# Performance work log

Hardware: AMD Instinct MI355X
Metric: run time of the kernel (lower is better)

The kernel has to match this reference:

```python
import jax, jax.numpy as jnp
import numpy as np

# Module constants (match init_kwargs / DCNv4 defaults)
N, C, H, W = 4, 256, 128, 128
G = 4                       # DCNv4 default group
KS = 3                      # kernel_size
K = KS * KS                 # 9 sampling points per group
Cg = C // G                 # channels per group
PAD_OFF = int(np.ceil(G * K * 3 / 8) * 8)  # 112, padded offset_mask dim
EPS = 1e-5                  # BatchNorm2d eps


def setup_inputs() -> dict:
    key = jax.random.key(0)
    ks = jax.random.split(key, 6)
    s = 0.05
    return {
        "x": jax.random.normal(ks[0], (N, C, H, W), jnp.float32),
        "conv_w": jax.random.normal(ks[1], (C, C, 1, 1), jnp.float32) * s,
        "bn1_gamma": jnp.ones((C,), jnp.float32),
        "bn1_beta": jnp.zeros((C,), jnp.float32),
        "bn1_mean": jnp.zeros((C,), jnp.float32),
        "bn1_var": jnp.ones((C,), jnp.float32),
        "value_w": jax.random.normal(ks[2], (C, C), jnp.float32) * s,
        "value_b": jnp.zeros((C,), jnp.float32),
        "offset_w": jax.random.normal(ks[3], (PAD_OFF, C), jnp.float32) * s,
        "offset_b": jnp.zeros((PAD_OFF,), jnp.float32),
        "out_w": jax.random.normal(ks[4], (C, C), jnp.float32) * s,
        "out_b": jnp.zeros((C,), jnp.float32),
        "bn2_gamma": jnp.ones((C,), jnp.float32),
        "bn2_beta": jnp.zeros((C,), jnp.float32),
        "bn2_mean": jnp.zeros((C,), jnp.float32),
        "bn2_var": jnp.ones((C,), jnp.float32),
    }


def _bilinear(v, lh, lw):
    """Bilinear sample v:(N,H,W,G,Cg) at float locs lh/lw:(N,H,W,G); zero outside."""
    n, h, w, g, c = v.shape
    h0 = jnp.floor(lh)
    w0 = jnp.floor(lw)
    dh = lh - h0
    dw = lw - w0
    h0i = h0.astype(jnp.int32)
    w0i = w0.astype(jnp.int32)
    vf = v.reshape(n, h * w, g, c)

    def gather(hh, ww):
        valid = (hh >= 0) & (hh < h) & (ww >= 0) & (ww < w)
        idx = jnp.clip(hh, 0, h - 1) * w + jnp.clip(ww, 0, w - 1)
        out = jnp.take_along_axis(vf, idx.reshape(n, h * w, g)[..., None], axis=1)
        return out.reshape(n, h, w, g, c) * valid[..., None].astype(v.dtype)

    w00 = (1 - dh) * (1 - dw)
    w01 = (1 - dh) * dw
    w10 = dh * (1 - dw)
    w11 = dh * dw
    return (gather(h0i, w0i) * w00[..., None]
            + gather(h0i, w0i + 1) * w01[..., None]
            + gather(h0i + 1, w0i) * w10[..., None]
            + gather(h0i + 1, w0i + 1) * w11[..., None])


def _bn(x_nchw, gamma, beta, mean, var):
    scale = (gamma / jnp.sqrt(var + EPS))[None, :, None, None]
    return x_nchw * scale + (beta - mean * gamma / jnp.sqrt(var + EPS))[None, :, None, None]


def reference(x, conv_w, bn1_gamma, bn1_beta, bn1_mean, bn1_var,
              value_w, value_b, offset_w, offset_b, out_w, out_b,
              bn2_gamma, bn2_beta, bn2_mean, bn2_var):
    n, _, h, w = x.shape
    # ---- Conv(c1,c2,k=1): 1x1 conv (no bias) + BN + SiLU ----
    y = jnp.einsum('nchw,oc->nohw', x, conv_w[:, :, 0, 0])
    y = jax.nn.silu(_bn(y, bn1_gamma, bn1_beta, bn1_mean, bn1_var))

    # ---- DCNv4 on (N, L, C) tokens ----
    t = y.transpose(0, 2, 3, 1)                      # (N,H,W,C)
    v = t @ value_w.T + value_b                      # value_proj
    om = t @ offset_w.T + offset_b                   # (N,H,W,112)
    om = om[..., : G * K * 3].reshape(n, h, w, G, K * 3)
    off = om[..., : 2 * K].reshape(n, h, w, G, K, 2) # (dx, dy) per point
    mask = om[..., 2 * K:]                           # (N,H,W,G,K), no softmax in v4
    v = v.reshape(n, h, w, G, Cg)

    hi = jnp.arange(h, dtype=jnp.float32)[None, :, None, None]
    wi = jnp.arange(w, dtype=jnp.float32)[None, None, :, None]
    out = jnp.zeros_like(v)
    for k in range(K):  # fixed small kernel loop (9 points)
        i, j = divmod(k, KS)
        lh = hi + (i - 1) + off[..., k, 1]           # stride=1, pad=1, dil=1
        lw = wi + (j - 1) + off[..., k, 0]           # offset_scale=1.0
        out = out + mask[..., k, None] * _bilinear(v, lh, lw)

    o = out.reshape(n, h, w, C) @ out_w.T + out_b    # output_proj
    o = o.transpose(0, 3, 1, 2)                      # back to NCHW

    # ---- final BN + SiLU ----
    return jax.nn.silu(_bn(o, bn2_gamma, bn2_beta, bn2_mean, bn2_var))
```

## Files before the change

### kernel.cpp

```cpp
#include <hip/hip_runtime.h>
#include <cstdint>

typedef unsigned short u16;
typedef unsigned int   u32;
typedef __attribute__((ext_vector_type(8))) __bf16 bf16x8;
typedef __attribute__((ext_vector_type(2))) float  f32x2;
typedef __attribute__((ext_vector_type(4))) float  f32x4;
typedef __attribute__((ext_vector_type(4))) u32    u32x4;

#define N_IMG 4
#define C_DIM 256
#define H_DIM 128
#define W_DIM 128
#define HW    (H_DIM * W_DIM)
#define M_TOT (N_IMG * HW)
#define CG    64
#define PADOFF 112
#define NCAT  368
#define EPSV  1e-5f

__device__ __forceinline__ u16 f2b(float f) {
  u32 u = __float_as_uint(f);
  u += 0x7fffu + ((u >> 16) & 1u);
  return (u16)(u >> 16);
}

__device__ __forceinline__ void async_cp16(const void* g, void* l) {
  __builtin_amdgcn_global_load_lds(
      (const __attribute__((address_space(1))) void*)g,
      (__attribute__((address_space(3))) void*)l, 16, 0, 0);
}

__global__ __launch_bounds__(256) void cast_all(
    const float* __restrict__ a0, u16* __restrict__ o0,
    const float* __restrict__ a1, u16* __restrict__ o1,
    const float* __restrict__ a2, u16* __restrict__ o2,
    const float* __restrict__ a3, u16* __restrict__ o3) {
  int i = blockIdx.x * 256 + threadIdx.x;
  const float* in; u16* out; int base;
  if (i < 16384)      { in = a0; out = o0; base = 0; }
  else if (i < 32768) { in = a1; out = o1; base = 16384; }
  else if (i < 39936) { in = a2; out = o2; base = 32768; }
  else                { in = a3; out = o3; base = 39936; }
  int j = i - base;
  f32x4 v = reinterpret_cast<const f32x4*>(in)[j];
  u32 lo = (u32)f2b(v[0]) | ((u32)f2b(v[1]) << 16);
  u32 hi = (u32)f2b(v[2]) | ((u32)f2b(v[3]) << 16);
  reinterpret_cast<u32*>(out)[2 * j]     = lo;
  reinterpret_cast<u32*>(out)[2 * j + 1] = hi;
}

__global__ __launch_bounds__(256) void fused_proj(
    const float* __restrict__ X, const u16* __restrict__ Bc,
    const u16* __restrict__ Wcat,
    u16* __restrict__ Vv, float* __restrict__ Om,
    const float* __restrict__ vbias, const float* __restrict__ obias,
    const float* __restrict__ gamma, const float* __restrict__ beta,
    const float* __restrict__ mean, const float* __restrict__ var) {
  constexpr int BM = 128, BK = 32;
  __shared__ __align__(16) u16 T[BM * C_DIM];
  __shared__ __align__(16) u16 As[BM * BK];
  __shared__ __align__(16) u16 Bs[BM * BK];
  const int tid  = threadIdx.x;
  const int lane = tid & 63;
  const int wave = tid >> 6;
  const int quad = lane >> 4;
  const int l16  = lane & 15;
  const int bm = blockIdx.x * BM;
  const int wm = (wave & 1) * 64;
  const int wn = (wave >> 1) * 64;
  const int img = bm >> 14;
  const int hw0 = bm & (HW - 1);
  const int p2  = (tid & 63) * 2;
  const int hh  = tid >> 6;
  const float* xb = X + (size_t)img * C_DIM * HW + hw0 + p2;

  for (int ny = 0; ny < 2; ++ny) {
    const int bn = ny * 128;
    f32x4 acc[4][4] = {};
    for (int ko = 0; ko < C_DIM; ko += BK) {
      float a0[8], a1[8];
#pragma unroll
      for (int j = 0; j < 8; ++j) {
        f32x2 fv = *reinterpret_cast<const f32x2*>(
            xb + (size_t)(ko + hh * 8 + j) * HW);
        a0[j] = fv.x; a1[j] = fv.y;
      }
      u32x4 w0, w1;
#pragma unroll
      for (int j = 0; j < 4; ++j) {
        w0[j] = (u32)f2b(a0[2 * j]) | ((u32)f2b(a0[2 * j + 1]) << 16);
        w1[j] = (u32)f2b(a1[2 * j]) | ((u32)f2b(a1[2 * j + 1]) << 16);
      }
      {
        u32x4* Ar = reinterpret_cast<u32x4*>(As);
        int sw = hh ^ ((p2 >> 1) & 3);
        Ar[p2 * 4 + sw]       = w0;
        Ar[(p2 + 1) * 4 + sw] = w1;
      }
#pragma unroll
      for (int it = 0; it < 2; ++it) {
        int chunk = it * 256 + tid;
        int r  = chunk >> 2;
        int kk = (chunk & 3) << 3;
        async_cp16(Bc + (size_t)(bn + r) * C_DIM + (ko + kk),
                   Bs + (size_t)(it * 256 + wave * 64) * 8);
      }
      __syncthreads();
      const bf16x8* Apf = reinterpret_cast<const bf16x8*>(As);
      const bf16x8* Bpf = reinterpret_cast<const bf16x8*>(Bs);
      bf16x8 af[4], bfr[4];
#pragma unroll
      for (int mi = 0; mi < 4; ++mi) {
        int r = wm + mi * 16 + l16;
        af[mi] = Apf[r * 4 + (quad ^ ((r >> 1) & 3))];
      }
#pragma unroll
      for (int ni = 0; ni < 4; ++ni)
        bfr[ni] = Bpf[(wn + ni * 16 + l16) * 4 + quad];
#pragma unroll
      for (int mi = 0; mi < 4; ++mi)
#pragma unroll
        for (int ni = 0; ni < 4; ++ni)
          acc[mi][ni] = __builtin_amdgcn_mfma_f32_16x16x32_bf16(
              af[mi], bfr[ni], acc[mi][ni], 0, 0, 0);
      __syncthreads();
    }
#pragma unroll
    for (int ni = 0; ni < 4; ++ni) {
      int n = bn + wn + ni * 16 + l16;
      float sc = gamma[n] * rsqrtf(var[n] + EPSV);
      float sh = beta[n] - mean[n] * sc;
#pragma unroll
      for (int mi = 0; mi < 4; ++mi) {
        int row = wm + mi * 16 + quad * 4;
#pragma unroll
        for (int i = 0; i < 4; ++i) {
          float y = acc[mi][ni][i] * sc + sh;
          y = y / (1.f + __expf(-y));
          int rr = row + i;
          T[rr * C_DIM + (((n >> 3) ^ (rr & 15)) << 3) + (n & 7)] = f2b(y);
        }
      }
    }
  }
  __syncthreads();

  for (int nc = 0; nc < 3; ++nc) {
    const int n0 = nc * 128;
    f32x4 acc[4][4] = {};
    for (int ko = 0; ko < C_DIM; ko += BK) {
#pragma unroll
      for (int it = 0; it < 2; ++it) {
        int chunk = it * 256 + tid;
        int r  = chunk >> 2;
        int kk = (chunk & 3) << 3;
        int br = n0 + r; if (br >= NCAT) br = NCAT - 1;
        async_cp16(Wcat + (size_t)br * C_DIM + (ko + kk),
                   Bs + (size_t)(it * 256 + wave * 64) * 8);
      }
      __syncthreads();
      const bf16x8* Bpf = reinterpret_cast<const bf16x8*>(Bs);
      bf16x8 af[4], bfr[4];
#pragma unroll
      for (int mi = 0; mi < 4; ++mi) {
        int row = wm + mi * 16 + l16;
        int ch  = (ko >> 3) + quad;
        af[mi] = *reinterpret_cast<const bf16x8*>(
            &T[row * C_DIM + ((ch ^ (row & 15)) << 3)]);
      }
#pragma unroll
      for (int ni = 0; ni < 4; ++ni)
        bfr[ni] = Bpf[(wn + ni * 16 + l16) * 4 + quad];
#pragma unroll
      for (int mi = 0; mi < 4; ++mi)
#pragma unroll
        for (int ni = 0; ni < 4; ++ni)
          acc[mi][ni] = __builtin_amdgcn_mfma_f32_16x16x32_bf16(
              af[mi], bfr[ni], acc[mi][ni], 0, 0, 0);
      __syncthreads();
    }
#pragma unroll
    for (int ni = 0; ni < 4; ++ni) {
      int n = n0 + wn + ni * 16 + l16;
      if (n < C_DIM) {
        float sh = vbias[n];
#pragma unroll
        for (int mi = 0; mi < 4; ++mi) {
          int mrow = bm + wm + mi * 16 + quad * 4;
#pragma unroll
          for (int i = 0; i < 4; ++i)
            Vv[(size_t)(mrow + i) * C_DIM + n] = f2b(acc[mi][ni][i] + sh);
        }
      } else {
        int col = n - C_DIM;
        bool ok = col < PADOFF;
        float sh = ok ? obias[col] : 0.f;
#pragma unroll
        for (int mi = 0; mi < 4; ++mi) {
          int mrow = bm + wm + mi * 16 + quad * 4;
#pragma unroll
          for (int i = 0; i < 4; ++i)
            if (ok) Om[(size_t)(mrow + i) * PADOFF + col] = acc[mi][ni][i] + sh;
        }
      }
    }
  }
}

__global__ __launch_bounds__(256) void gemm_out(
    const u16* __restrict__ A, const u16* __restrict__ B,
    float* __restrict__ Cf,
    const float* __restrict__ bias,
    const float* __restrict__ gamma, const float* __restrict__ beta,
    const float* __restrict__ mean, const float* __restrict__ var) {
  constexpr int BM = 128, BK = 64;
  __shared__ __align__(16) u16 As[BM * BK];
  __shared__ __align__(16) u16 Bs[BM * BK];
  const int tid  = threadIdx.x;
  const int lane = tid & 63;
  const int wave = tid >> 6;
  const int quad = lane >> 4;
  const int l16  = lane & 15;
  const int bm = blockIdx.x * BM;
  const int bn = blockIdx.y * BM;
  const int wm = (wave & 1) * 64;
  const int wn = (wave >> 1) * 64;

  f32x4 acc[4][4] = {};

  for (int ko = 0; ko < C_DIM; ko += BK) {
#pragma unroll
    for (int it = 0; it < 4; ++it) {
      int chunk = it * 256 + tid;
      int r  = chunk >> 3;
      int j  = chunk & 7;
      int kk = (j ^ (r & 7)) << 3;
      async_cp16(A + (size_t)(bm + r) * C_DIM + (ko + kk),
                 As + (size_t)(it * 256 + wave * 64) * 8);
      async_cp16(B + (size_t)(bn + r) * C_DIM + (ko + kk),
                 Bs + (size_t)(it * 256 + wave * 64) * 8);
    }
    __syncthreads();
    const bf16x8* Ap = reinterpret_cast<const bf16x8*>(As);
    const bf16x8* Bp = reinterpret_cast<const bf16x8*>(Bs);
#pragma unroll
    for (int ks = 0; ks < 2; ++ks) {
      bf16x8 af[4], bfr[4];
#pragma unroll
      for (int mi = 0; mi < 4; ++mi) {
        int row = wm + mi * 16 + l16;
        af[mi] = Ap[row * 8 + ((ks * 4 + quad) ^ (row & 7))];
      }
#pragma unroll
      for (int ni = 0; ni < 4; ++ni) {
        int row = wn + ni * 16 + l16;
        bfr[ni] = Bp[row * 8 + ((ks * 4 + quad) ^ (row & 7))];
      }
#pragma unroll
      for (int mi = 0; mi < 4; ++mi)
#pragma unroll
        for (int ni = 0; ni < 4; ++ni)
          acc[mi][ni] = __builtin_amdgcn_mfma_f32_16x16x32_bf16(
              af[mi], bfr[ni], acc[mi][ni], 0, 0, 0);
    }
    __syncthreads();
  }

#pragma unroll
  for (int ni = 0; ni < 4; ++ni) {
    int n = bn + wn + ni * 16 + l16;
    float sc = gamma[n] * rsqrtf(var[n] + EPSV);
    float sh = beta[n] - mean[n] * sc + bias[n] * sc;
#pragma unroll
    for (int mi = 0; mi < 4; ++mi) {
      int mrow = bm + wm + mi * 16 + quad * 4;
      int img = mrow >> 14;
      int hw  = mrow & (HW - 1);
      f32x4 y;
#pragma unroll
      for (int i = 0; i < 4; ++i) {
        float z = acc[mi][ni][i] * sc + sh;
        y[i] = z / (1.f + __expf(-z));
      }
      *reinterpret_cast<f32x4*>(
          Cf + (size_t)img * C_DIM * HW + (size_t)n * HW + hw) = y;
    }
  }
}

__global__ __launch_bounds__(256) void dcn_sample(
    const u16* __restrict__ v, const float* __restrict__ om,
    u16* __restrict__ outp) {
  __shared__ float sm[16 * PADOFF];
  const int tid = threadIdx.x;
  const int bid = blockIdx.x;
  const int cpx = gridDim.x >> 3;
  const int wg  = (bid & 7) * cpx + (bid >> 3);
  const int m0  = wg * 16;
  {
    const float* src = om + (size_t)m0 * PADOFF;
#pragma unroll
    for (int i = 0; i < 7; ++i) sm[tid + i * 256] = src[tid + i * 256];
  }
  __syncthreads();
  const int c4 = tid & 3;
  const int g  = (tid >> 2) & 3;
  const int pl = tid >> 4;
  const int m  = m0 + pl;
  const int n  = m >> 14;
  const int hw = m & (HW - 1);
  const int h = hw >> 7, w = hw & 127;
  const float* p = sm + pl * PADOFF + g * 27;
  const u16* vb = v + (size_t)n * HW * C_DIM + g * CG + c4 * 16;
  float acc[16] = {};
#pragma unroll
  for (int k = 0; k < 9; ++k) {
    const int di = k / 3 - 1, dj = k % 3 - 1;
    float ox = p[2 * k], oy = p[2 * k + 1], mk = p[18 + k];
    float lh = (float)(h + di) + oy;
    float lw = (float)(w + dj) + ox;
    float fh = floorf(lh), fw = floorf(lw);
    float dh = lh - fh, dw = lw - fw;
    int h0 = (int)fh, w0 = (int)fw;
    float wy0 = (1.f - dh) * mk, wy1 = dh * mk;
    float wx0 = 1.f - dw, wx1 = dw;
    bool okw0 = (u32)w0 < (u32)W_DIM;
    bool okw1 = (u32)(w0 + 1) < (u32)W_DIM;
    int w0c = min(max(w0, 0), W_DIM - 1);
    int w1c = min(max(w0 + 1, 0), W_DIM - 1);
#pragma unroll
    for (int cy = 0; cy < 2; ++cy) {
      int hh = h0 + cy;
      bool okh = (u32)hh < (u32)H_DIM;
      int hc = min(max(hh, 0), H_DIM - 1);
      const u16* rowp = vb + (size_t)(hc << 7) * C_DIM;
      const u16* qA = rowp + (size_t)w0c * C_DIM;
      const u16* qB = rowp + (size_t)w1c * C_DIM;
      u32x4 a0 = *reinterpret_cast<const u32x4*>(qA);
      u32x4 a1 = *reinterpret_cast<const u32x4*>(qA + 8);
      u32x4 b0 = *reinterpret_cast<const u32x4*>(qB);
      u32x4 b1 = *reinterpret_cast<const u32x4*>(qB + 8);
      float wyc = (cy == 0) ? wy0 : wy1;
      float wtA = (okh && okw0) ? wyc * wx0 : 0.f;
      float wtB = (okh && okw1) ? wyc * wx1 : 0.f;
      u32 wp;
      asm("v_cvt_pk_bf16_f32 %0, %1, %2" : "=v"(wp) : "v"(wtA), "v"(wtB));
#pragma unroll
      for (int j = 0; j < 4; ++j) {
        u32 lo0 = __builtin_amdgcn_perm(a0[j], b0[j], 0x01000504u);
        u32 hi0 = __builtin_amdgcn_perm(a0[j], b0[j], 0x03020706u);
        u32 lo1 = __builtin_amdgcn_perm(a1[j], b1[j], 0x01000504u);
        u32 hi1 = __builtin_amdgcn_perm(a1[j], b1[j], 0x03020706u);
        asm("v_dot2_f32_bf16 %0, %1, %2, %3"
            : "=v"(acc[2 * j]) : "v"(lo0), "v"(wp), "v"(acc[2 * j]));
        asm("v_dot2_f32_bf16 %0, %1, %2, %3"
            : "=v"(acc[2 * j + 1]) : "v"(hi0), "v"(wp), "v"(acc[2 * j + 1]));
        asm("v_dot2_f32_bf16 %0, %1, %2, %3"
            : "=v"(acc[8 + 2 * j]) : "v"(lo1), "v"(wp), "v"(acc[8 + 2 * j]));
        asm("v_dot2_f32_bf16 %0, %1, %2, %3"
            : "=v"(acc[8 + 2 * j + 1]) : "v"(hi1), "v"(wp), "v"(acc[8 + 2 * j + 1]));
      }
    }
  }
  u32x4 r0, r1;
#pragma unroll
  for (int j = 0; j < 4; ++j) {
    u32 pa, pb;
    asm("v_cvt_pk_bf16_f32 %0, %1, %2"
        : "=v"(pa) : "v"(acc[2 * j]), "v"(acc[2 * j + 1]));
    asm("v_cvt_pk_bf16_f32 %0, %1, %2"
        : "=v"(pb) : "v"(acc[8 + 2 * j]), "v"(acc[8 + 2 * j + 1]));
    r0[j] = pa; r1[j] = pb;
  }
  u16* o = outp + (size_t)m * C_DIM + g * CG + c4 * 16;
  *reinterpret_cast<u32x4*>(o)     = r0;
  *reinterpret_cast<u32x4*>(o + 8) = r1;
}

extern "C" void kernel_launch(void* const* d_in, const int* in_sizes, int n_in,
                              void* d_out, int out_size, void* d_ws, size_t ws_size,
                              hipStream_t stream) {
  const float* x        = (const float*)d_in[0];
  const float* conv_w   = (const float*)d_in[1];
  const float* bn1_g    = (const float*)d_in[2];
  const float* bn1_b    = (const float*)d_in[3];
  const float* bn1_m    = (const float*)d_in[4];
  const float* bn1_v    = (const float*)d_in[5];
  const float* value_w  = (const float*)d_in[6];
  const float* value_b  = (const float*)d_in[7];
  const float* offset_w = (const float*)d_in[8];
  const float* offset_b = (const float*)d_in[9];
  const float* out_w    = (const float*)d_in[10];
  const float* out_b    = (const float*)d_in[11];
  const float* bn2_g    = (const float*)d_in[12];
  const float* bn2_b    = (const float*)d_in[13];
  const float* bn2_m    = (const float*)d_in[14];
  const float* bn2_v    = (const float*)d_in[15];

  char* ws = (char*)d_ws;
  u16*   vv   = (u16*)(ws);
  float* om   = (float*)(ws + 33554432);
  u16*   dcn  = (u16*)(ws + 67108864);
  u16*   wc   = (u16*)(ws + 100663296);
  u16*   wcat = (u16*)(ws + 100794368);
  u16*   wout = (u16*)(ws + 100982784);
  float* outp = (float*)d_out;

  cast_all<<<220, 256, 0, stream>>>(conv_w, wc, value_w, wcat,
                                    offset_w, wcat + 65536, out_w, wout);

  fused_proj<<<dim3(M_TOT / 128), 256, 0, stream>>>(
      x, wc, wcat, vv, om, value_b, offset_b,
      bn1_g, bn1_b, bn1_m, bn1_v);
  dcn_sample<<<dim3(M_TOT / 16), 256, 0, stream>>>(vv, om, dcn);
  gemm_out<<<dim3(M_TOT / 128, 2), 256, 0, stream>>>(
      dcn, wout, outp, out_b, bn2_g, bn2_b, bn2_m, bn2_v);
}
```

Baseline: 254.9 us.

## Load X once for both conv halves and double-buffer stage-two weight tiles

The first GEMM now streams and converts the fp32 input tile once per K step and feeds both 128-column halves, using two accumulator sets instead of reading X twice. The second GEMM reuses the As and Bs buffers as a ping-pong pair, prefetching the next Wcat tile with async copies while computing the current one, synchronised by explicit vmcnt waits and barriers. Launch bounds now request two blocks per CU. The extra accumulators raise register pressure and may cause spills under the two-block occupancy cap.

New measurement: 260.7 us. 2.3% more time.

```diff
diff --git a/kernel.cpp b/kernel.cpp
--- a/kernel.cpp
+++ b/kernel.cpp
@@ -50,7 +50,7 @@
   reinterpret_cast<u32*>(out)[2 * j + 1] = hi;
 }
 
-__global__ __launch_bounds__(256) void fused_proj(
+__global__ __launch_bounds__(256, 2) void fused_proj(
     const float* __restrict__ X, const u16* __restrict__ Bc,
     const u16* __restrict__ Wcat,
     u16* __restrict__ Vv, float* __restrict__ Om,
@@ -75,46 +75,47 @@
   const int hh  = tid >> 6;
   const float* xb = X + (size_t)img * C_DIM * HW + hw0 + p2;
 
-  for (int ny = 0; ny < 2; ++ny) {
-    const int bn = ny * 128;
-    f32x4 acc[4][4] = {};
-    for (int ko = 0; ko < C_DIM; ko += BK) {
-      float a0[8], a1[8];
-#pragma unroll
-      for (int j = 0; j < 8; ++j) {
-        f32x2 fv = *reinterpret_cast<const f32x2*>(
-            xb + (size_t)(ko + hh * 8 + j) * HW);
-        a0[j] = fv.x; a1[j] = fv.y;
-      }
-      u32x4 w0, w1;
-#pragma unroll
-      for (int j = 0; j < 4; ++j) {
-        w0[j] = (u32)f2b(a0[2 * j]) | ((u32)f2b(a0[2 * j + 1]) << 16);
-        w1[j] = (u32)f2b(a1[2 * j]) | ((u32)f2b(a1[2 * j + 1]) << 16);
-      }
-      {
-        u32x4* Ar = reinterpret_cast<u32x4*>(As);
-        int sw = hh ^ ((p2 >> 1) & 3);
-        Ar[p2 * 4 + sw]       = w0;
-        Ar[(p2 + 1) * 4 + sw] = w1;
-      }
-#pragma unroll
-      for (int it = 0; it < 2; ++it) {
-        int chunk = it * 256 + tid;
-        int r  = chunk >> 2;
-        int kk = (chunk & 3) << 3;
-        async_cp16(Bc + (size_t)(bn + r) * C_DIM + (ko + kk),
-                   Bs + (size_t)(it * 256 + wave * 64) * 8);
-      }
-      __syncthreads();
-      const bf16x8* Apf = reinterpret_cast<const bf16x8*>(As);
-      const bf16x8* Bpf = reinterpret_cast<const bf16x8*>(Bs);
-      bf16x8 af[4], bfr[4];
-#pragma unroll
-      for (int mi = 0; mi < 4; ++mi) {
-        int r = wm + mi * 16 + l16;
-        af[mi] = Apf[r * 4 + (quad ^ ((r >> 1) & 3))];
-      }
+  f32x4 acc0[4][4] = {};
+  f32x4 acc1[4][4] = {};
+  for (int ko = 0; ko < C_DIM; ko += BK) {
+    float a0[8], a1[8];
+#pragma unroll
+    for (int j = 0; j < 8; ++j) {
+      f32x2 fv = *reinterpret_cast<const f32x2*>(
+          xb + (size_t)(ko + hh * 8 + j) * HW);
+      a0[j] = fv.x; a1[j] = fv.y;
+    }
+    u32x4 w0, w1;
+#pragma unroll
+    for (int j = 0; j < 4; ++j) {
+      w0[j] = (u32)f2b(a0[2 * j]) | ((u32)f2b(a0[2 * j + 1]) << 16);
+      w1[j] = (u32)f2b(a1[2 * j]) | ((u32)f2b(a1[2 * j + 1]) << 16);
+    }
+    {
+      u32x4* Ar = reinterpret_cast<u32x4*>(As);
+      int sw = hh ^ ((p2 >> 1) & 3);
+      Ar[p2 * 4 + sw]       = w0;
+      Ar[(p2 + 1) * 4 + sw] = w1;
+    }
+#pragma unroll
+    for (int it = 0; it < 2; ++it) {
+      int chunk = it * 256 + tid;
+      int r  = chunk >> 2;
+      int kk = (chunk & 3) << 3;
+      async_cp16(Bc + (size_t)r * C_DIM + (ko + kk),
+                 Bs + (size_t)(it * 256 + wave * 64) * 8);
+    }
+    __syncthreads();
+    const bf16x8* Apf = reinterpret_cast<const bf16x8*>(As);
+    const bf16x8* Bpf = reinterpret_cast<const bf16x8*>(Bs);
+    bf16x8 af[4];
+#pragma unroll
+    for (int mi = 0; mi < 4; ++mi) {
+      int r = wm + mi * 16 + l16;
+      af[mi] = Apf[r * 4 + (quad ^ ((r >> 1) & 3))];
+    }
+    {
+      bf16x8 bfr[4];
 #pragma unroll
       for (int ni = 0; ni < 4; ++ni)
         bfr[ni] = Bpf[(wn + ni * 16 + l16) * 4 + quad];
@@ -122,10 +123,34 @@
       for (int mi = 0; mi < 4; ++mi)
 #pragma unroll
         for (int ni = 0; ni < 4; ++ni)
-          acc[mi][ni] = __builtin_amdgcn_mfma_f32_16x16x32_bf16(
-              af[mi], bfr[ni], acc[mi][ni], 0, 0, 0);
-      __syncthreads();
-    }
+          acc0[mi][ni] = __builtin_amdgcn_mfma_f32_16x16x32_bf16(
+              af[mi], bfr[ni], acc0[mi][ni], 0, 0, 0);
+    }
+    __syncthreads();
+#pragma unroll
+    for (int it = 0; it < 2; ++it) {
+      int chunk = it * 256 + tid;
+      int r  = chunk >> 2;
+      int kk = (chunk & 3) << 3;
+      async_cp16(Bc + (size_t)(128 + r) * C_DIM + (ko + kk),
+                 Bs + (size_t)(it * 256 + wave * 64) * 8);
+    }
+    __syncthreads();
+    {
+      bf16x8 bfr[4];
+#pragma unroll
+      for (int ni = 0; ni < 4; ++ni)
+        bfr[ni] = Bpf[(wn + ni * 16 + l16) * 4 + quad];
+#pragma unroll
+      for (int mi = 0; mi < 4; ++mi)
+#pragma unroll
+        for (int ni = 0; ni < 4; ++ni)
+          acc1[mi][ni] = __builtin_amdgcn_mfma_f32_16x16x32_bf16(
+              af[mi], bfr[ni], acc1[mi][ni], 0, 0, 0);
+    }
+    __syncthreads();
+  }
+  auto epi1 = [&](f32x4 (&acc)[4][4], int bn) {
 #pragma unroll
     for (int ni = 0; ni < 4; ++ni) {
       int n = bn + wn + ni * 16 + l16;
@@ -143,29 +168,44 @@
         }
       }
     }
-  }
+  };
+  epi1(acc0, 0);
+  epi1(acc1, 128);
   __syncthreads();
 
+  auto stage2 = [&](u16* buf, int n0, int ko) {
+#pragma unroll
+    for (int it = 0; it < 2; ++it) {
+      int chunk = it * 256 + tid;
+      int r  = chunk >> 2;
+      int kk = (chunk & 3) << 3;
+      int br = n0 + r; if (br >= NCAT) br = NCAT - 1;
+      async_cp16(Wcat + (size_t)br * C_DIM + (ko + kk),
+                 buf + (size_t)(it * 256 + wave * 64) * 8);
+    }
+  };
   for (int nc = 0; nc < 3; ++nc) {
     const int n0 = nc * 128;
     f32x4 acc[4][4] = {};
-    for (int ko = 0; ko < C_DIM; ko += BK) {
-#pragma unroll
-      for (int it = 0; it < 2; ++it) {
-        int chunk = it * 256 + tid;
-        int r  = chunk >> 2;
-        int kk = (chunk & 3) << 3;
-        int br = n0 + r; if (br >= NCAT) br = NCAT - 1;
-        async_cp16(Wcat + (size_t)br * C_DIM + (ko + kk),
-                   Bs + (size_t)(it * 256 + wave * 64) * 8);
-      }
-      __syncthreads();
-      const bf16x8* Bpf = reinterpret_cast<const bf16x8*>(Bs);
+    stage2(As, n0, 0);
+    for (int koi = 0; koi < 8; ++koi) {
+      const u16* cur = (koi & 1) ? Bs : As;
+      u16*       nxt = (koi & 1) ? As : Bs;
+      if (koi < 7) {
+        stage2(nxt, n0, (koi + 1) * BK);
+        asm volatile("s_waitcnt vmcnt(2)" ::: "memory");
+      } else {
+        asm volatile("s_waitcnt vmcnt(0)" ::: "memory");
+      }
+      __builtin_amdgcn_sched_barrier(0);
+      __builtin_amdgcn_s_barrier();
+      __builtin_amdgcn_sched_barrier(0);
+      const bf16x8* Bpf = reinterpret_cast<const bf16x8*>(cur);
       bf16x8 af[4], bfr[4];
 #pragma unroll
       for (int mi = 0; mi < 4; ++mi) {
         int row = wm + mi * 16 + l16;
-        int ch  = (ko >> 3) + quad;
+        int ch  = koi * 4 + quad;
         af[mi] = *reinterpret_cast<const bf16x8*>(
             &T[row * C_DIM + ((ch ^ (row & 15)) << 3)]);
       }
@@ -178,7 +218,8 @@
         for (int ni = 0; ni < 4; ++ni)
           acc[mi][ni] = __builtin_amdgcn_mfma_f32_16x16x32_bf16(
               af[mi], bfr[ni], acc[mi][ni], 0, 0, 0);
-      __syncthreads();
+      __builtin_amdgcn_sched_barrier(0);
+      __builtin_amdgcn_s_barrier();
     }
 #pragma unroll
     for (int ni = 0; ni < 4; ++ni) {
```
